# Optimization experiments

Hardware: AMD Instinct MI355X
Metric: run time of the kernel (lower is better)

The kernel has to match this reference:

```python
import jax, jax.numpy as jnp
import numpy as np

B, N, F, G = 2, 8, 32, 32
EPS = 1e-8
elu = jax.nn.elu

def pconv(x, w, b):
    # pointwise Conv3d (1x1x1): x (..., C, D, H, W), w (O, C), b (O,)
    return jnp.einsum('...cdhw,oc->...odhw', x, w) + b[:, None, None, None]

def mean_var(x, weight):
    # weighted mean/variance over the num_images axis (axis=1), keepdims
    mean = jnp.sum(x * weight, axis=1, keepdims=True)
    var = jnp.sum(weight * (x - mean) ** 2, axis=1, keepdims=True)
    return mean, var

def setup_inputs() -> dict:
    key = jax.random.key(0)
    ks = jax.random.split(key, 20)
    def wmat(k, o, i):
        return jax.random.normal(k, (o, i), jnp.float32) * (1.0 / np.sqrt(i))
    return {
        'features': jax.random.normal(ks[0], (B, N, F, G, G, G), jnp.float32),
        'mask': jax.random.uniform(ks[1], (B, N, 1, G, G, G), jnp.float32),
        'voxel_depth': jax.random.normal(ks[2], (B, N, 1, G, G, G), jnp.float32),
        'voxel_dir': jax.random.normal(ks[3], (B, N, 3, G, G, G), jnp.float32),
        'rde_w1': wmat(ks[4], F // 2, 4), 'rde_b1': jnp.zeros((F // 2,), jnp.float32),
        'rde_w2': wmat(ks[5], F, F // 2), 'rde_b2': jnp.zeros((F,), jnp.float32),
        'base_w1': wmat(ks[6], 2 * F, 3 * F), 'base_b1': jnp.zeros((2 * F,), jnp.float32),
        'base_w2': wmat(ks[7], F, 2 * F), 'base_b2': jnp.zeros((F,), jnp.float32),
        'vis_w1': wmat(ks[8], F, F), 'vis_b1': jnp.zeros((F,), jnp.float32),
        'vis_w2': wmat(ks[9], F + 1, F), 'vis_b2': jnp.zeros((F + 1,), jnp.float32),
        'vis2_w1': wmat(ks[10], F, F), 'vis2_b1': jnp.zeros((F,), jnp.float32),
        'vis2_w2': wmat(ks[11], 1, F), 'vis2_b2': jnp.zeros((1,), jnp.float32),
        'stat_w': wmat(ks[12], F, 2 * F + 1), 'stat_b': jnp.zeros((F,), jnp.float32),
    }

def reference(features, mask, voxel_depth, voxel_dir,
              rde_w1, rde_b1, rde_w2, rde_b2,
              base_w1, base_b1, base_w2, base_b2,
              vis_w1, vis_b1, vis_w2, vis_b2,
              vis2_w1, vis2_b1, vis2_w2, vis2_b2,
              stat_w, stat_b):
    b, n = features.shape[:2]
    # ray/depth encoder (pointwise MLP over 4 channels)
    rde = jnp.concatenate([voxel_dir, voxel_depth], axis=2)  # (B,N,4,G,G,G)
    rde = elu(pconv(elu(pconv(rde, rde_w1, rde_b1)), rde_w2, rde_b2))
    feats = features + rde
    # mask-normalized weights over views
    weight = mask / (jnp.sum(mask, axis=1, keepdims=True) + EPS)
    mean, var = mean_var(feats, weight)
    gf = jnp.concatenate([mean, var], axis=2)  # (B,1,2F,G,G,G)
    x = jnp.concatenate([jnp.broadcast_to(gf, (b, n) + gf.shape[2:]), feats], axis=2)  # (B,N,3F,...)
    x = elu(pconv(elu(pconv(x, base_w1, base_b1)), base_w2, base_b2))
    xv = elu(pconv(elu(pconv(x * weight, vis_w1, vis_b1)), vis_w2, vis_b2))
    x_res, vis = xv[:, :, :-1], xv[:, :, -1:]
    vis = jax.nn.sigmoid(vis) * mask
    x = x + x_res
    vis = jax.nn.sigmoid(pconv(elu(pconv(x * vis, vis2_w1, vis2_b1)), vis2_w2, vis2_b2)) * mask
    weight = vis / (jnp.sum(vis, axis=1, keepdims=True) + EPS)
    mean, var = mean_var(x, weight)
    gf = jnp.concatenate([mean[:, 0], var[:, 0], jnp.mean(weight, axis=1)], axis=1)  # (B,2F+1,G,G,G)
    return elu(pconv(gf, stat_w, stat_b))  # (B,F,G,G,G)
```

## Files before the change

### kernel.cpp

```cpp
#include <hip/hip_runtime.h>


#define G3 32768
#define KP 104

typedef _Float16 h8 __attribute__((ext_vector_type(8)));
typedef _Float16 h4 __attribute__((ext_vector_type(4)));
typedef _Float16 h2 __attribute__((ext_vector_type(2)));
typedef float f4 __attribute__((ext_vector_type(4)));
typedef float f2 __attribute__((ext_vector_type(2)));
typedef float f4a __attribute__((ext_vector_type(4), aligned(4)));

#define WB() __builtin_amdgcn_wave_barrier()

__device__ __forceinline__ float eluf(float x) {
    return x > 0.0f ? x : __expf(x) - 1.0f;
}
__device__ __forceinline__ float sigmoidf(float x) {
    return 1.0f / (1.0f + __expf(-x));
}
__device__ __forceinline__ float red8v(float v) {
    v += __shfl_xor(v, 8, 64);
    v += __shfl_xor(v, 16, 64);
    v += __shfl_xor(v, 32, 64);
    return v;
}

#define WS_BW1 0
#define WS_BW2 6144
#define WS_VW1 8192
#define WS_VW2 9216
#define WS_V2W1 10752

__global__ void prep_kernel(const float* __restrict__ bw1,
                            const float* __restrict__ bw2,
                            const float* __restrict__ vw1,
                            const float* __restrict__ vw2,
                            const float* __restrict__ v2w1,
                            _Float16* __restrict__ wh) {
    int t = blockIdx.x * blockDim.x + threadIdx.x;
    int stride = gridDim.x * blockDim.x;
    for (int i = t; i < 6144; i += stride) wh[WS_BW1 + i] = (_Float16)bw1[i];
    for (int i = t; i < 2048; i += stride) wh[WS_BW2 + i] = (_Float16)bw2[i];
    for (int i = t; i < 1024; i += stride) wh[WS_VW1 + i] = (_Float16)vw1[i];
    for (int i = t; i < 1536; i += stride)
        wh[WS_VW2 + i] = (i < 1056) ? (_Float16)vw2[i] : (_Float16)0.0f;
    for (int i = t; i < 1024; i += stride) wh[WS_V2W1 + i] = (_Float16)v2w1[i];
}

template <int K, int KS, int MT>
__device__ __forceinline__ void mfma_pass(const _Float16* __restrict__ Wf,
                                          const _Float16* __restrict__ Y,
                                          int srck0, int pass, int lane,
                                          f4 acc[2][4]) {
    const int q = lane >> 4, nlo = lane & 15;
    h8 bf[2][KS];
#pragma unroll
    for (int j = 0; j < 2; ++j) {
        const _Float16* yc =
            Y + ((pass * 2 + j) * 16 + nlo) * KP + srck0 + q * 8;
#pragma unroll
        for (int kt = 0; kt < KS; ++kt) bf[j][kt] = *(const h8*)(yc + kt * 32);
    }
#pragma unroll
    for (int mt = 0; mt < MT; ++mt) {
        h8 af[KS];
#pragma unroll
        for (int kt = 0; kt < KS; ++kt)
            af[kt] = *(const h8*)(Wf + (mt * 16 + nlo) * K + q * 8 + kt * 32);
#pragma unroll
        for (int j = 0; j < 2; ++j)
#pragma unroll
            for (int kt = 0; kt < KS; ++kt)
                acc[j][mt] = __builtin_amdgcn_mfma_f32_16x16x32_f16(
                    af[kt], bf[j][kt], acc[j][mt], 0, 0, 0);
    }
}

template <int MT>
__device__ __forceinline__ void epi_pass(f4 acc[2][4],
                                         const float* __restrict__ bias,
                                         _Float16* __restrict__ Y, int dstk0,
                                         int pass, int lane) {
    const int q = lane >> 4, nlo = lane & 15;
#pragma unroll
    for (int j = 0; j < 2; ++j) {
        const int col = (pass * 2 + j) * 16 + nlo;
#pragma unroll
        for (int mt = 0; mt < MT; ++mt) {
            f4 bb = *(const f4*)(bias + mt * 16 + q * 4);
            h4 hv;
#pragma unroll
            for (int r = 0; r < 4; ++r)
                hv[r] = (_Float16)eluf(acc[j][mt][r] + bb[r]);
            *(h4*)(Y + col * KP + dstk0 + mt * 16 + q * 4) = hv;
        }
    }
}

__global__ __launch_bounds__(64) void ibr_mfma(
    const float* __restrict__ features, const float* __restrict__ mask,
    const float* __restrict__ vdepth, const float* __restrict__ vdir,
    const float* __restrict__ rde_w1, const float* __restrict__ rde_b1,
    const float* __restrict__ rde_w2, const float* __restrict__ rde_b2,
    const float* __restrict__ base_b1, const float* __restrict__ base_b2,
    const float* __restrict__ vis_b1, const float* __restrict__ vis_b2,
    const float* __restrict__ vis2_b1, const float* __restrict__ vis2_w2,
    const float* __restrict__ vis2_b2, const float* __restrict__ stat_w,
    const float* __restrict__ stat_b, const _Float16* __restrict__ wh,
    float* __restrict__ out) {
    __shared__ _Float16 Y[64 * KP];

#define GAPF(col) ((float*)(Y + (col)*KP + 96))

    const int lane = threadIdx.x;
    const int n = lane >> 3, vi = lane & 7;
    const int blk = blockIdx.x;
    const int b = blk >> 12;
    const int i = blk & 4095;
    const int v0 = (((i & 7) << 9) | (i >> 3)) << 3;
    const int bn = b * 8 + n;
    const int v = v0 + vi;

    const float m = mask[bn * G3 + v];
    const float r0 = vdir[(bn * 3 + 0) * G3 + v];
    const float r1 = vdir[(bn * 3 + 1) * G3 + v];
    const float r2 = vdir[(bn * 3 + 2) * G3 + v];
    const float r3 = vdepth[bn * G3 + v];
    float f[32];
#pragma unroll
    for (int c = 0; c < 32; ++c) f[c] = features[(bn * 32 + c) * G3 + v];

    float h16[16];
#pragma unroll
    for (int o = 0; o < 16; ++o) {
        float a = rde_b1[o] + rde_w1[o * 4 + 0] * r0 + rde_w1[o * 4 + 1] * r1 +
                  rde_w1[o * 4 + 2] * r2 + rde_w1[o * 4 + 3] * r3;
        h16[o] = eluf(a);
    }
#pragma unroll
    for (int o = 0; o < 32; ++o) {
        float a = rde_b2[o];
#pragma unroll
        for (int c = 0; c < 16; ++c) a += rde_w2[o * 16 + c] * h16[c];
        f[o] += eluf(a);
    }

    const float msum = red8v(m);
    const float invA = 1.0f / (msum + 1e-8f);
    const float wt = m * invA;
    const float sA = msum * invA;
    {
        f2 mw = {m, wt};
        *(f2*)GAPF(lane) = mw;
    }

    {
        _Float16* yl = Y + lane * KP + 64;
#pragma unroll
        for (int g = 0; g < 4; ++g) {
            h8 t;
#pragma unroll
            for (int e = 0; e < 8; ++e) t[e] = (_Float16)f[g * 8 + e];
            *(h8*)(yl + g * 8) = t;
        }
    }
    WB();

    {
        const int pv = lane >> 3, u = lane & 7;
        const float kA = 2.0f - __shfl(sA, pv, 64);
#pragma unroll
        for (int t2 = 0; t2 < 2; ++t2) {
            const int dw = u + 8 * t2;
            float s0 = 0.f, s1 = 0.f, q0 = 0.f, q1 = 0.f;
#pragma unroll
            for (int nn = 0; nn < 8; ++nn) {
                const int col = nn * 8 + pv;
                h2 xv = *(const h2*)(Y + col * KP + 64 + dw * 2);
                const float wv = GAPF(col)[1];
                const float x0 = (float)xv[0], x1 = (float)xv[1];
                s0 += wv * x0; q0 += wv * x0 * x0;
                s1 += wv * x1; q1 += wv * x1 * x1;
            }
            h2 hm = {(_Float16)s0, (_Float16)s1};
            h2 hv = {(_Float16)(q0 - s0 * s0 * kA),
                     (_Float16)(q1 - s1 * s1 * kA)};
#pragma unroll
            for (int nn = 0; nn < 8; ++nn) {
                *(h2*)(Y + (nn * 8 + pv) * KP + dw * 2) = hm;
                *(h2*)(Y + (nn * 8 + pv) * KP + 32 + dw * 2) = hv;
            }
        }
    }
    WB();

#pragma unroll
    for (int pass = 0; pass < 2; ++pass) {
        f4 acc[2][4] = {};
        mfma_pass<96, 3, 4>(wh + WS_BW1, Y, 0, pass, lane, acc);
        epi_pass<4>(acc, base_b1, Y, 0, pass, lane);
    }
    WB();

#pragma unroll
    for (int pass = 0; pass < 2; ++pass) {
        f4 acc[2][4] = {};
        mfma_pass<64, 2, 2>(wh + WS_BW2, Y, 0, pass, lane, acc);
        const int q = lane >> 4, nlo = lane & 15;
#pragma unroll
        for (int j = 0; j < 2; ++j) {
            const int col = (pass * 2 + j) * 16 + nlo;
            const float w = GAPF(col)[1];
#pragma unroll
            for (int mt = 0; mt < 2; ++mt) {
                f4 bb = *(const f4*)(base_b2 + mt * 16 + q * 4);
                h4 hx, hxw;
#pragma unroll
                for (int r = 0; r < 4; ++r) {
                    const float xv = eluf(acc[j][mt][r] + bb[r]);
                    hx[r] = (_Float16)xv;
                    hxw[r] = (_Float16)(xv * w);
                }
                *(h4*)(Y + col * KP + 64 + mt * 16 + q * 4) = hx;
                *(h4*)(Y + col * KP + mt * 16 + q * 4) = hxw;
            }
        }
    }
    WB();

#pragma unroll
    for (int pass = 0; pass < 2; ++pass) {
        f4 acc[2][4] = {};
        mfma_pass<32, 1, 2>(wh + WS_VW1, Y, 0, pass, lane, acc);
        epi_pass<2>(acc, vis_b1, Y, 32, pass, lane);
    }
    WB();

#pragma unroll
    for (int pass = 0; pass < 2; ++pass) {
        f4 acc[2][4] = {};
        mfma_pass<32, 1, 3>(wh + WS_VW2, Y, 32, pass, lane, acc);
        const int q = lane >> 4, nlo = lane & 15;
#pragma unroll
        for (int j = 0; j < 2; ++j) {
            const int col = (pass * 2 + j) * 16 + nlo;
#pragma unroll
            for (int mt = 0; mt < 2; ++mt) {
                f4 bb = *(const f4*)(vis_b2 + mt * 16 + q * 4);
                h4 hv;
#pragma unroll
                for (int r = 0; r < 4; ++r)
                    hv[r] = (_Float16)eluf(acc[j][mt][r] + bb[r]);
                *(h4*)(Y + col * KP + mt * 16 + q * 4) = hv;
            }
            if (q == 0) {
                const float vv = acc[j][2][0] + vis_b2[32];
                GAPF(col)[2] = sigmoidf(eluf(vv)) * GAPF(col)[0];
            }
        }
    }
    WB();

    {
        const int pv = lane >> 3, u = lane & 7;
#pragma unroll
        for (int nn = 0; nn < 8; ++nn) {
            const int col = nn * 8 + pv;
            const float vn = GAPF(col)[2];
#pragma unroll
            for (int t2 = 0; t2 < 2; ++t2) {
                const int dw = u + 8 * t2;
                h2 xr = *(const h2*)(Y + col * KP + dw * 2);
                h2 xo = *(const h2*)(Y + col * KP + 64 + dw * 2);
                const float x0 = (float)xo[0] + (float)xr[0];
                const float x1 = (float)xo[1] + (float)xr[1];
                h2 hx = {(_Float16)x0, (_Float16)x1};
                h2 hxv = {(_Float16)(x0 * vn), (_Float16)(x1 * vn)};
                *(h2*)(Y + col * KP + 64 + dw * 2) = hx;
                *(h2*)(Y + col * KP + dw * 2) = hxv;
            }
        }
    }
    WB();

#pragma unroll
    for (int pass = 0; pass < 2; ++pass) {
        f4 acc[2][4] = {};
        mfma_pass<32, 1, 2>(wh + WS_V2W1, Y, 0, pass, lane, acc);
        epi_pass<2>(acc, vis2_b1, Y, 32, pass, lane);
    }
    WB();

    float sCl;
    {
        const _Float16* yc = Y + lane * KP + 32;
        float a0 = vis2_b2[0], a1 = 0.f;
#pragma unroll
        for (int t = 0; t < 16; ++t) {
            h2 p = *(const h2*)(yc + t * 2);
            if (t & 1)
                a1 += vis2_w2[t * 2] * (float)p[0] +
                      vis2_w2[t * 2 + 1] * (float)p[1];
            else
                a0 += vis2_w2[t * 2] * (float)p[0] +
                      vis2_w2[t * 2 + 1] * (float)p[1];
        }
        const float visv = sigmoidf(a0 + a1) * m;
        const float b0 = red8v(visv);
        const float invC = 1.0f / (b0 + 1e-8f);
        GAPF(lane)[3] = visv * invC;
        sCl = b0 * invC;
    }
    WB();

    {
        const int pv = lane >> 3, u = lane & 7;
        const float kC = 2.0f - __shfl(sCl, pv, 64);
#pragma unroll
        for (int t2 = 0; t2 < 2; ++t2) {
            const int dw = u + 8 * t2;
            float s0 = 0.f, s1 = 0.f, q0 = 0.f, q1 = 0.f;
#pragma unroll
            for (int nn = 0; nn < 8; ++nn) {
                const int col = nn * 8 + pv;
                h2 xv = *(const h2*)(Y + col * KP + 64 + dw * 2);
                const float wv = GAPF(col)[3];
                const float x0 = (float)xv[0], x1 = (float)xv[1];
                s0 += wv * x0; q0 += wv * x0 * x0;
                s1 += wv * x1; q1 += wv * x1 * x1;
            }
            f2 mp = {s0, s1};
            f2 vp = {q0 - s0 * s0 * kC, q1 - s1 * s1 * kC};
            *(f2*)((float*)(Y + (2 * pv) * KP) + dw * 2) = mp;
            *(f2*)((float*)(Y + (2 * pv + 1) * KP) + dw * 2) = vp;
        }
    }
    WB();

    {
        const int o = lane >> 1;
        const int vi0 = (lane & 1) * 4;
        const float wm_own = sCl * 0.125f;
        const float* row = stat_w + o * 65;
        float wmv[4];
#pragma unroll
        for (int k2 = 0; k2 < 4; ++k2) wmv[k2] = __shfl(wm_own, vi0 + k2, 64);
        float pr[4];
#pragma unroll
        for (int k2 = 0; k2 < 4; ++k2) pr[k2] = stat_b[o];
#pragma unroll
        for (int c4 = 0; c4 < 8; ++c4) {
            f4a wr = *(const f4a*)(row + c4 * 4);
            f4a ur = *(const f4a*)(row + 32 + c4 * 4);
#pragma unroll
            for (int k2 = 0; k2 < 4; ++k2) {
                const float* sm = (const float*)(Y + (2 * (vi0 + k2)) * KP);
                const float* sv = (const float*)(Y + (2 * (vi0 + k2) + 1) * KP);
                f4 a = *(const f4*)(sm + c4 * 4);
                f4 bvv = *(const f4*)(sv + c4 * 4);
                pr[k2] += wr[0] * a[0] + wr[1] * a[1] + wr[2] * a[2] +
                          wr[3] * a[3] + ur[0] * bvv[0] + ur[1] * bvv[1] +
                          ur[2] * bvv[2] + ur[3] * bvv[3];
            }
        }
        const float wl = row[64];
        f4 res;
#pragma unroll
        for (int k2 = 0; k2 < 4; ++k2)
            res[k2] = eluf(pr[k2] + wl * wmv[k2]);
        *(f4*)(out + ((b * 32 + o) << 15) + v0 + vi0) = res;
    }
#undef GAPF
}

extern "C" void kernel_launch(void* const* d_in, const int* in_sizes, int n_in,
                              void* d_out, int out_size, void* d_ws,
                              size_t ws_size, hipStream_t stream) {
    const float* features = (const float*)d_in[0];
    const float* mask = (const float*)d_in[1];
    const float* vdepth = (const float*)d_in[2];
    const float* vdir = (const float*)d_in[3];
    const float* rde_w1 = (const float*)d_in[4];
    const float* rde_b1 = (const float*)d_in[5];
    const float* rde_w2 = (const float*)d_in[6];
    const float* rde_b2 = (const float*)d_in[7];
    const float* base_w1 = (const float*)d_in[8];
    const float* base_b1 = (const float*)d_in[9];
    const float* base_w2 = (const float*)d_in[10];
    const float* base_b2 = (const float*)d_in[11];
    const float* vis_w1 = (const float*)d_in[12];
    const float* vis_b1 = (const float*)d_in[13];
    const float* vis_w2 = (const float*)d_in[14];
    const float* vis_b2 = (const float*)d_in[15];
    const float* vis2_w1 = (const float*)d_in[16];
    const float* vis2_b1 = (const float*)d_in[17];
    const float* vis2_w2 = (const float*)d_in[18];
    const float* vis2_b2 = (const float*)d_in[19];
    const float* stat_w = (const float*)d_in[20];
    const float* stat_b = (const float*)d_in[21];

    _Float16* wh = (_Float16*)d_ws;
    prep_kernel<<<24, 256, 0, stream>>>(base_w1, base_w2, vis_w1, vis_w2,
                                        vis2_w1, wh);

    ibr_mfma<<<8192, 64, 0, stream>>>(
        features, mask, vdepth, vdir, rde_w1, rde_b1, rde_w2, rde_b2, base_b1,
        base_b2, vis_b1, vis_b2, vis2_b1, vis2_w2, vis2_b2, stat_w, stat_b, wh,
        (float*)d_out);
}
```

Measured before the change: 203.9 us.

## Compute view-invariant mean/var part of base_w1 once per voxel, shrink LDS tile

Splits base_w1 into a global-feature part and a per-view feature part. The mean/var contribution is identical across the 8 views of a voxel, so it is computed once per voxel with a compact MFMA and added in the epilogue. The per-view GEMM then only has K=32 instead of K=96. This lets the LDS row pitch shrink from 104 to 80 halves, and launch bounds now request 4 waves per EU for occupancy. In exchange the LDS layout is reshuffled throughout, and the stat stage uses new indexing that must stay consistent.

```diff
diff --git a/kernel.cpp b/kernel.cpp
--- a/kernel.cpp
+++ b/kernel.cpp
@@ -2,7 +2,7 @@
 
 
 #define G3 32768
-#define KP 104
+#define KP 80
 
 typedef _Float16 h8 __attribute__((ext_vector_type(8)));
 typedef _Float16 h4 __attribute__((ext_vector_type(4)));
@@ -26,7 +26,8 @@
     return v;
 }
 
-#define WS_BW1 0
+#define WS_BW1G 0
+#define WS_BW1F 4096
 #define WS_BW2 6144
 #define WS_VW1 8192
 #define WS_VW2 9216
@@ -40,7 +41,14 @@
                             _Float16* __restrict__ wh) {
     int t = blockIdx.x * blockDim.x + threadIdx.x;
     int stride = gridDim.x * blockDim.x;
-    for (int i = t; i < 6144; i += stride) wh[WS_BW1 + i] = (_Float16)bw1[i];
+    for (int i = t; i < 4096; i += stride) {
+        int o = i >> 6, k = i & 63;
+        wh[WS_BW1G + i] = (_Float16)bw1[o * 96 + k];
+    }
+    for (int i = t; i < 2048; i += stride) {
+        int o = i >> 5, k = i & 31;
+        wh[WS_BW1F + i] = (_Float16)bw1[o * 96 + 64 + k];
+    }
     for (int i = t; i < 2048; i += stride) wh[WS_BW2 + i] = (_Float16)bw2[i];
     for (int i = t; i < 1024; i += stride) wh[WS_VW1 + i] = (_Float16)vw1[i];
     for (int i = t; i < 1536; i += stride)
@@ -98,7 +106,7 @@
     }
 }
 
-__global__ __launch_bounds__(64) void ibr_mfma(
+__global__ __launch_bounds__(64, 4) void ibr_mfma(
     const float* __restrict__ features, const float* __restrict__ mask,
     const float* __restrict__ vdepth, const float* __restrict__ vdir,
     const float* __restrict__ rde_w1, const float* __restrict__ rde_b1,
@@ -111,7 +119,7 @@
     float* __restrict__ out) {
     __shared__ _Float16 Y[64 * KP];
 
-#define GAPF(col) ((float*)(Y + (col)*KP + 96))
+#define GAPF(col) ((float*)(Y + (col)*KP + 72))
 
     const int lane = threadIdx.x;
     const int n = lane >> 3, vi = lane & 7;
@@ -156,7 +164,7 @@
     }
 
     {
-        _Float16* yl = Y + lane * KP + 64;
+        _Float16* yl = Y + lane * KP;
 #pragma unroll
         for (int g = 0; g < 4; ++g) {
             h8 t;
@@ -177,7 +185,7 @@
 #pragma unroll
             for (int nn = 0; nn < 8; ++nn) {
                 const int col = nn * 8 + pv;
-                h2 xv = *(const h2*)(Y + col * KP + 64 + dw * 2);
+                h2 xv = *(const h2*)(Y + col * KP + dw * 2);
                 const float wv = GAPF(col)[1];
                 const float x0 = (float)xv[0], x1 = (float)xv[1];
                 s0 += wv * x0; q0 += wv * x0 * x0;
@@ -186,20 +194,51 @@
             h2 hm = {(_Float16)s0, (_Float16)s1};
             h2 hv = {(_Float16)(q0 - s0 * s0 * kA),
                      (_Float16)(q1 - s1 * s1 * kA)};
-#pragma unroll
-            for (int nn = 0; nn < 8; ++nn) {
-                *(h2*)(Y + (nn * 8 + pv) * KP + dw * 2) = hm;
-                *(h2*)(Y + (nn * 8 + pv) * KP + 32 + dw * 2) = hv;
-            }
-        }
-    }
-    WB();
-
-#pragma unroll
-    for (int pass = 0; pass < 2; ++pass) {
-        f4 acc[2][4] = {};
-        mfma_pass<96, 3, 4>(wh + WS_BW1, Y, 0, pass, lane, acc);
-        epi_pass<4>(acc, base_b1, Y, 0, pass, lane);
+            _Float16* g =
+                Y + (pv * 8 + (dw >> 2)) * KP + 64 + ((2 * dw) & 7);
+            *(h2*)g = hm;
+            *(h2*)(g + 4 * KP) = hv;
+        }
+    }
+    WB();
+
+    {
+        const int q = lane >> 4, nlo = lane & 15, vox = nlo & 7;
+        f4 accgf[4] = {};
+        {
+            h8 bg0 = *(const h8*)(Y + (vox * 8 + q) * KP + 64);
+            h8 bg1 = *(const h8*)(Y + (vox * 8 + 4 + q) * KP + 64);
+#pragma unroll
+            for (int mt = 0; mt < 4; ++mt) {
+                h8 a0 =
+                    *(const h8*)(wh + WS_BW1G + (mt * 16 + nlo) * 64 + q * 8);
+                h8 a1 = *(const h8*)(wh + WS_BW1G + (mt * 16 + nlo) * 64 +
+                                     q * 8 + 32);
+                accgf[mt] = __builtin_amdgcn_mfma_f32_16x16x32_f16(
+                    a0, bg0, accgf[mt], 0, 0, 0);
+                accgf[mt] = __builtin_amdgcn_mfma_f32_16x16x32_f16(
+                    a1, bg1, accgf[mt], 0, 0, 0);
+            }
+        }
+#pragma unroll
+        for (int pass = 0; pass < 2; ++pass) {
+            f4 acc[2][4] = {};
+            mfma_pass<32, 1, 4>(wh + WS_BW1F, Y, 0, pass, lane, acc);
+#pragma unroll
+            for (int j = 0; j < 2; ++j) {
+                const int col = (pass * 2 + j) * 16 + nlo;
+#pragma unroll
+                for (int mt = 0; mt < 4; ++mt) {
+                    f4 bb = *(const f4*)(base_b1 + mt * 16 + q * 4);
+                    h4 hv;
+#pragma unroll
+                    for (int r = 0; r < 4; ++r)
+                        hv[r] =
+                            (_Float16)eluf(acc[j][mt][r] + accgf[mt][r] + bb[r]);
+                    *(h4*)(Y + col * KP + mt * 16 + q * 4) = hv;
+                }
+            }
+        }
     }
     WB();
 
@@ -222,7 +261,7 @@
                     hx[r] = (_Float16)xv;
                     hxw[r] = (_Float16)(xv * w);
                 }
-                *(h4*)(Y + col * KP + 64 + mt * 16 + q * 4) = hx;
+                *(h4*)(Y + col * KP + 32 + mt * 16 + q * 4) = hx;
                 *(h4*)(Y + col * KP + mt * 16 + q * 4) = hxw;
             }
         }
@@ -233,14 +272,14 @@
     for (int pass = 0; pass < 2; ++pass) {
         f4 acc[2][4] = {};
         mfma_pass<32, 1, 2>(wh + WS_VW1, Y, 0, pass, lane, acc);
-        epi_pass<2>(acc, vis_b1, Y, 32, pass, lane);
+        epi_pass<2>(acc, vis_b1, Y, 0, pass, lane);
     }
     WB();
 
 #pragma unroll
     for (int pass = 0; pass < 2; ++pass) {
         f4 acc[2][4] = {};
-        mfma_pass<32, 1, 3>(wh + WS_VW2, Y, 32, pass, lane, acc);
+        mfma_pass<32, 1, 3>(wh + WS_VW2, Y, 0, pass, lane, acc);
         const int q = lane >> 4, nlo = lane & 15;
 #pragma unroll
         for (int j = 0; j < 2; ++j) {
@@ -272,12 +311,12 @@
             for (int t2 = 0; t2 < 2; ++t2) {
                 const int dw = u + 8 * t2;
                 h2 xr = *(const h2*)(Y + col * KP + dw * 2);
-                h2 xo = *(const h2*)(Y + col * KP + 64 + dw * 2);
+                h2 xo = *(const h2*)(Y + col * KP + 32 + dw * 2);
                 const float x0 = (float)xo[0] + (float)xr[0];
                 const float x1 = (float)xo[1] + (float)xr[1];
                 h2 hx = {(_Float16)x0, (_Float16)x1};
                 h2 hxv = {(_Float16)(x0 * vn), (_Float16)(x1 * vn)};
-                *(h2*)(Y + col * KP + 64 + dw * 2) = hx;
+                *(h2*)(Y + col * KP + 32 + dw * 2) = hx;
                 *(h2*)(Y + col * KP + dw * 2) = hxv;
             }
         }
@@ -288,13 +327,13 @@
     for (int pass = 0; pass < 2; ++pass) {
         f4 acc[2][4] = {};
         mfma_pass<32, 1, 2>(wh + WS_V2W1, Y, 0, pass, lane, acc);
-        epi_pass<2>(acc, vis2_b1, Y, 32, pass, lane);
+        epi_pass<2>(acc, vis2_b1, Y, 0, pass, lane);
     }
     WB();
 
     float sCl;
     {
-        const _Float16* yc = Y + lane * KP + 32;
+        const _Float16* yc = Y + lane * KP;
         float a0 = vis2_b2[0], a1 = 0.f;
 #pragma unroll
         for (int t = 0; t < 16; ++t) {
@@ -324,7 +363,7 @@
 #pragma unroll
             for (int nn = 0; nn < 8; ++nn) {
                 const int col = nn * 8 + pv;
-                h2 xv = *(const h2*)(Y + col * KP + 64 + dw * 2);
+                h2 xv = *(const h2*)(Y + col * KP + 32 + dw * 2);
                 const float wv = GAPF(col)[3];
                 const float x0 = (float)xv[0], x1 = (float)xv[1];
                 s0 += wv * x0; q0 += wv * x0 * x0;
@@ -332,8 +371,8 @@
             }
             f2 mp = {s0, s1};
             f2 vp = {q0 - s0 * s0 * kC, q1 - s1 * s1 * kC};
-            *(f2*)((float*)(Y + (2 * pv) * KP) + dw * 2) = mp;
-            *(f2*)((float*)(Y + (2 * pv + 1) * KP) + dw * 2) = vp;
+            *(f2*)((float*)(Y + (4 * pv + t2) * KP) + 2 * u) = mp;
+            *(f2*)((float*)(Y + (4 * pv + 2 + t2) * KP) + 2 * u) = vp;
         }
     }
     WB();
@@ -355,10 +394,14 @@
             f4a ur = *(const f4a*)(row + 32 + c4 * 4);
 #pragma unroll
             for (int k2 = 0; k2 < 4; ++k2) {
-                const float* sm = (const float*)(Y + (2 * (vi0 + k2)) * KP);
-                const float* sv = (const float*)(Y + (2 * (vi0 + k2) + 1) * KP);
-                f4 a = *(const f4*)(sm + c4 * 4);
-                f4 bvv = *(const f4*)(sv + c4 * 4);
+                const float* sm =
+                    (const float*)(Y + (4 * (vi0 + k2) + (c4 >> 2)) * KP) +
+                    (c4 & 3) * 4;
+                const float* sv =
+                    (const float*)(Y + (4 * (vi0 + k2) + 2 + (c4 >> 2)) * KP) +
+                    (c4 & 3) * 4;
+                f4 a = *(const f4*)sm;
+                f4 bvv = *(const f4*)sv;
                 pr[k2] += wr[0] * a[0] + wr[1] * a[1] + wr[2] * a[2] +
                           wr[3] * a[3] + ur[0] * bvv[0] + ur[1] * bvv[1] +
                           ur[2] * bvv[2] + ur[3] * bvv[3];
```

Measured after the change: 195.7 us. -4.0%, faster.
